# Kernel optimization log

Measured on AMD Instinct MI355X. Metric: run time of the kernel, lower is better.

## Reference

```python
import jax, jax.numpy as jnp
import numpy as np

B, N, C, H = 8, 2048, 512, 8
D = C // H  # head_dim = 64

def rope(t):
    # t: (B, H, T, D); rotate even/odd interleaved pairs
    T = t.shape[2]
    inv_freq = 1.0 / (10000.0 ** (jnp.arange(0, D, 2, dtype=t.dtype) / D))  # (D/2,)
    pos = jnp.arange(T, dtype=t.dtype)
    freqs = pos[:, None] * inv_freq[None, :]            # (T, D/2)
    cos, sin = jnp.cos(freqs), jnp.sin(freqs)           # broadcast over (B,H)
    t_un = t[..., 0::2]
    t_ev = t[..., 1::2]
    r_un = t_un * cos - t_ev * sin
    r_ev = t_un * sin + t_ev * cos
    # interleave back: (..., D/2, 2) -> (..., D)
    return jnp.stack([r_un, r_ev], axis=-1).reshape(t.shape)

def setup_inputs() -> dict:
    key = jax.random.key(0)
    k1, k2, k3, k4 = jax.random.split(key, 4)
    x = jax.random.normal(k1, (B, N, C), dtype=jnp.float32)
    mask = jax.random.normal(k2, (B, N), dtype=jnp.float32)
    W_qkv = jax.random.normal(k3, (3 * C, C), dtype=jnp.float32) * (1.0 / np.sqrt(C))
    W_proj = jax.random.normal(k4, (C, C), dtype=jnp.float32) * (1.0 / np.sqrt(C))
    b_proj = jnp.zeros((C,), dtype=jnp.float32)
    return {"x": x, "mask": mask, "W_qkv": W_qkv, "W_proj": W_proj,
            "b_proj": b_proj, "num_cls_token": 1}

def reference(x, mask, W_qkv, W_proj, b_proj, num_cls_token):
    scale = D ** (-0.5)
    qkv = jnp.einsum('bnc,fc->bnf', x, W_qkv)             # (B,N,3C)
    qkv = qkv.reshape(B, N, 3, H, D).transpose(2, 0, 3, 1, 4)  # (3,B,H,N,D)
    q, k, v = qkv[0], qkv[1], qkv[2]
    nc = num_cls_token
    if nc > 0:
        q = jnp.concatenate([q[:, :, :nc], rope(q[:, :, nc:])], axis=2)
        k = jnp.concatenate([k[:, :, :nc], rope(k[:, :, nc:])], axis=2)
    else:
        q, k = rope(q), rope(k)
    attn = jnp.einsum('bhnd,bhmd->bhnm', q * scale, k)    # (B,H,N,N)
    attn = attn + mask[:, None, None, :] + mask[:, None, :, None]
    attn = jax.nn.softmax(attn, axis=-1)
    out = jnp.einsum('bhnm,bhmd->bhnd', attn, v)          # (B,H,N,D)
    out = out.transpose(0, 2, 1, 3).reshape(B, N, C)
    return out @ W_proj.T + b_proj
```

## Files before the change

kernel.cpp:

```cpp
#include <hip/hip_runtime.h>
#include <cmath>

#define BB 8
#define NN 2048
#define CC 512
#define HH 8
#define DD 64
#define FF 1536
#define MM (BB*NN)

typedef _Float16 half_t;
typedef __attribute__((ext_vector_type(8))) _Float16 half8;
typedef __attribute__((ext_vector_type(4))) _Float16 half4;
typedef __attribute__((ext_vector_type(4))) float floatx4;

#define LOG2E 1.44269504088896f

typedef const __attribute__((address_space(1))) unsigned int* gas_ptr;
typedef __attribute__((address_space(3))) unsigned int* las_ptr;
__device__ __forceinline__ void gld16(const half_t* g, half_t* l) {
  __builtin_amdgcn_global_load_lds((gas_ptr)g, (las_ptr)l, 16, 0, 0);
}

__global__ __launch_bounds__(256) void cvt_kernel(
    const float* __restrict__ s, half_t* __restrict__ d, int n8) {
  int i = blockIdx.x * 256 + threadIdx.x;
  if (i < n8) {
    float4 a = ((const float4*)s)[i * 2], b = ((const float4*)s)[i * 2 + 1];
    half8 h;
    h[0] = (half_t)a.x; h[1] = (half_t)a.y; h[2] = (half_t)a.z; h[3] = (half_t)a.w;
    h[4] = (half_t)b.x; h[5] = (half_t)b.y; h[6] = (half_t)b.z; h[7] = (half_t)b.w;
    ((half8*)d)[i] = h;
  }
}

__global__ __launch_bounds__(256) void qkv_mfma_kernel(
    const half_t* __restrict__ Ah,
    const half_t* __restrict__ Bh,
    const int*   __restrict__ ncp,
    half_t* __restrict__ Qh, half_t* __restrict__ Kh, half_t* __restrict__ Vt)
{
  __shared__ union {
    struct { half_t A[128 * 32]; half_t B[128 * 32]; } s;
    half_t T[4][64 * 68];
  } sm;

  const int tid  = threadIdx.x;
  const int wave = tid >> 6, lane = tid & 63;
  const int L15  = lane & 15, quad = lane >> 4;
  const int wm = (wave & 1) * 64, wn = (wave >> 1) * 64;
  const int m0 = blockIdx.x * 128;
  const int f0 = blockIdx.y * 128;

  const int srow = lane >> 2;
  const int scolh = (lane & 3) * 8;
  const half_t* Ag = Ah + (size_t)(m0 + wave * 16 + srow) * CC + scolh;
  const half_t* Bg = Bh + (size_t)(f0 + wave * 16 + srow) * CC + scolh;
  half_t* Al = &sm.s.A[(wave * 16) * 32];
  half_t* Bl = &sm.s.B[(wave * 16) * 32];

  floatx4 acc[4][4];
#pragma unroll
  for (int i = 0; i < 4; ++i)
#pragma unroll
    for (int j = 0; j < 4; ++j) acc[i][j] = (floatx4){0.f, 0.f, 0.f, 0.f};

  for (int k0 = 0; k0 < CC; k0 += 32) {
    __syncthreads();
    gld16(Ag + k0,            Al);
    gld16(Ag + k0 + 64 * CC,  Al + 64 * 32);
    gld16(Bg + k0,            Bl);
    gld16(Bg + k0 + 64 * CC,  Bl + 64 * 32);
    __syncthreads();
    half8 af[4], bf[4];
#pragma unroll
    for (int mi = 0; mi < 4; ++mi)
      af[mi] = *(const half8*)&sm.s.A[(wm + mi * 16 + L15) * 32 + quad * 8];
#pragma unroll
    for (int ni = 0; ni < 4; ++ni)
      bf[ni] = *(const half8*)&sm.s.B[(wn + ni * 16 + L15) * 32 + quad * 8];
#pragma unroll
    for (int mi = 0; mi < 4; ++mi)
#pragma unroll
      for (int ni = 0; ni < 4; ++ni)
        acc[mi][ni] = __builtin_amdgcn_mfma_f32_16x16x32_f16(af[mi], bf[ni], acc[mi][ni], 0, 0, 0);
  }

  const int which = f0 >> 9;
  const int b     = m0 >> 11;
  const int n_base = (m0 & 2047) + wm;

  if (which < 2) {
    const int nc = *ncp;
    half_t* dst = which ? Kh : Qh;
    const float qscale = which ? 1.0f : (0.125f * LOG2E);
#pragma unroll
    for (int ni = 0; ni < 4; ++ni) {
      const int f = f0 + wn + ni * 16 + L15;
      const int h = (f >> 6) & 7;
      const int d = f & 63;
      const float invf = __powf(10000.0f, -(float)(d & ~1) * (1.0f / 64.0f));
      const float sgn = (d & 1) ? 1.0f : -1.0f;
#pragma unroll
      for (int mi = 0; mi < 4; ++mi)
#pragma unroll
        for (int r = 0; r < 4; ++r) {
          const int n = n_base + mi * 16 + quad * 4 + r;
          float v = acc[mi][ni][r];
          float p = __shfl_xor(v, 1, 64);
          if (n >= nc) {
            float sv, cv;
            __sincosf((float)(n - nc) * invf, &sv, &cv);
            v = v * cv + sgn * p * sv;
          }
          dst[(((size_t)(b * HH + h) * NN + n) << 6) + d] = (half_t)(v * qscale);
        }
    }
  } else {
    __syncthreads();
#pragma unroll
    for (int ni = 0; ni < 4; ++ni)
#pragma unroll
      for (int mi = 0; mi < 4; ++mi)
#pragma unroll
        for (int r = 0; r < 4; ++r)
          sm.T[wave][(ni * 16 + L15) * 68 + mi * 16 + quad * 4 + r] = (half_t)acc[mi][ni][r];
    __syncthreads();
    const int h = ((f0 + wn) >> 6) & 7;
    const size_t gbase = ((size_t)(b * HH + h) * DD + lane) * NN + n_base;
#pragma unroll
    for (int c = 0; c < 8; ++c)
      *(half8*)(Vt + gbase + c * 8) = *(const half8*)&sm.T[wave][lane * 68 + c * 8];
  }
}

#define KPAD 72
#define PPAD 68
#define EXP2_OFF 4.3280851f
__global__ __launch_bounds__(256, 4) void flash_mfma_kernel(
    const half_t* __restrict__ Qh,
    const half_t* __restrict__ Kh,
    const half_t* __restrict__ Vt,
    const float*  __restrict__ mask,
    half_t* __restrict__ O)
{
  __shared__ half_t Ks[64 * KPAD];
  __shared__ half_t Vs[64 * KPAD];
  __shared__ half_t Ps[4][32 * PPAD];

  const int tid  = threadIdx.x;
  const int wave = tid >> 6;
  const int lane = tid & 63;
  const int L15  = lane & 15;
  const int quad = lane >> 4;

  const int bid  = blockIdx.x;
  const int xcd  = bid & 7;
  const int slot = bid >> 3;
  const int qt   = slot & 15;
  const int head = (slot >> 4) * 8 + xcd;
  const int b    = head >> 3;
  const int h    = head & 7;

  const half_t* Kt_base = Kh + ((((size_t)b * HH + h) * NN) << 6);
  const half_t* Vt_base = Vt + ((((size_t)b * HH + h) * DD) * NN);

  half8 qa[2][2];
#pragma unroll
  for (int g = 0; g < 2; ++g) {
    const half_t* Qrow =
        Qh + ((((size_t)b * HH + h) * NN + qt * 128 + wave * 32 + g * 16 + L15) << 6);
    qa[g][0] = *(const half8*)(Qrow + quad * 8);
    qa[g][1] = *(const half8*)(Qrow + 32 + quad * 8);
  }

  floatx4 oacc[2][4];
#pragma unroll
  for (int g = 0; g < 2; ++g)
#pragma unroll
    for (int sd = 0; sd < 4; ++sd) oacc[g][sd] = (floatx4){0.f, 0.f, 0.f, 0.f};
  float l_part[2][4] = {};

  const int sn = tid >> 3;
  const int sp = (tid & 7) * 8;
  half8 kreg[2], vreg[2];
  float mk_cur[4], mk_nxt[4];
#define LOAD_KV(kt)                                                               \
  {                                                                               \
    kreg[0] = *(const half8*)(Kt_base + (((size_t)(kt) * 64 + sn) << 6) + sp);    \
    kreg[1] = *(const half8*)(Kt_base + (((size_t)(kt) * 64 + sn + 32) << 6) + sp); \
    vreg[0] = *(const half8*)(Vt_base + (size_t)sn * NN + (kt) * 64 + sp);        \
    vreg[1] = *(const half8*)(Vt_base + (size_t)(sn + 32) * NN + (kt) * 64 + sp); \
  }
#define LOAD_MK(kt, dstm)                                                         \
  {                                                                               \
    _Pragma("unroll")                                                             \
    for (int s = 0; s < 4; ++s)                                                   \
      dstm[s] = mask[(size_t)b * NN + (kt) * 64 + s * 16 + L15] * LOG2E - EXP2_OFF; \
  }

  LOAD_KV(0)
  LOAD_MK(0, mk_cur)

  for (int kt = 0; kt < NN / 64; ++kt) {
    __syncthreads();
    *(half8*)&Ks[sn * KPAD + sp]        = kreg[0];
    *(half8*)&Ks[(sn + 32) * KPAD + sp] = kreg[1];
    *(half8*)&Vs[sn * KPAD + sp]        = vreg[0];
    *(half8*)&Vs[(sn + 32) * KPAD + sp] = vreg[1];
    __syncthreads();
    if (kt + 1 < NN / 64) {
      LOAD_KV(kt + 1)
      LOAD_MK(kt + 1, mk_nxt)
    }

    floatx4 S[2][4];
#pragma unroll
    for (int s = 0; s < 4; ++s) {
      half8 kb0 = *(const half8*)&Ks[(s * 16 + L15) * KPAD + quad * 8];
      half8 kb1 = *(const half8*)&Ks[(s * 16 + L15) * KPAD + 32 + quad * 8];
#pragma unroll
      for (int g = 0; g < 2; ++g) {
        floatx4 a = (floatx4){0.f, 0.f, 0.f, 0.f};
        a = __builtin_amdgcn_mfma_f32_16x16x32_f16(qa[g][0], kb0, a, 0, 0, 0);
        a = __builtin_amdgcn_mfma_f32_16x16x32_f16(qa[g][1], kb1, a, 0, 0, 0);
        S[g][s] = a;
      }
    }

#pragma unroll
    for (int g = 0; g < 2; ++g)
#pragma unroll
      for (int s = 0; s < 4; ++s)
#pragma unroll
        for (int r = 0; r < 4; ++r) {
          float p = __builtin_amdgcn_exp2f(S[g][s][r] + mk_cur[s]);
          l_part[g][r] += p;
          Ps[wave][(g * 16 + quad * 4 + r) * PPAD + s * 16 + L15] = (half_t)p;
        }

    half8 pa[2][2];
#pragma unroll
    for (int g = 0; g < 2; ++g) {
      pa[g][0] = *(const half8*)&Ps[wave][(g * 16 + L15) * PPAD + quad * 8];
      pa[g][1] = *(const half8*)&Ps[wave][(g * 16 + L15) * PPAD + 32 + quad * 8];
    }

#pragma unroll
    for (int sd = 0; sd < 4; ++sd) {
      half8 vb0 = *(const half8*)&Vs[(sd * 16 + L15) * KPAD + quad * 8];
      half8 vb1 = *(const half8*)&Vs[(sd * 16 + L15) * KPAD + 32 + quad * 8];
#pragma unroll
      for (int g = 0; g < 2; ++g) {
        oacc[g][sd] = __builtin_amdgcn_mfma_f32_16x16x32_f16(pa[g][0], vb0, oacc[g][sd], 0, 0, 0);
        oacc[g][sd] = __builtin_amdgcn_mfma_f32_16x16x32_f16(pa[g][1], vb1, oacc[g][sd], 0, 0, 0);
      }
    }

#pragma unroll
    for (int s = 0; s < 4; ++s) mk_cur[s] = mk_nxt[s];
  }

#pragma unroll
  for (int g = 0; g < 2; ++g)
#pragma unroll
    for (int r = 0; r < 4; ++r) {
#pragma unroll
      for (int off = 1; off < 16; off <<= 1)
        l_part[g][r] += __shfl_xor(l_part[g][r], off, 64);
    }

#pragma unroll
  for (int g = 0; g < 2; ++g)
#pragma unroll
    for (int r = 0; r < 4; ++r) {
      const float invl = 1.0f / l_part[g][r];
      const int row = qt * 128 + wave * 32 + g * 16 + quad * 4 + r;
#pragma unroll
      for (int sd = 0; sd < 4; ++sd)
        O[(((size_t)b * NN + row) << 9) + (h << 6) + sd * 16 + L15] =
            (half_t)(oacc[g][sd][r] * invl);
    }
}

__global__ __launch_bounds__(256) void proj_mfma_kernel(
    const half_t* __restrict__ Ah,
    const half_t* __restrict__ Bh,
    const float* __restrict__ bias,
    float* __restrict__ out)
{
  __shared__ half_t As[128 * 32];
  __shared__ half_t Bs[128 * 32];

  const int tid  = threadIdx.x;
  const int wave = tid >> 6, lane = tid & 63;
  const int L15  = lane & 15, quad = lane >> 4;
  const int wm = (wave & 1) * 64, wn = (wave >> 1) * 64;
  const int m0 = blockIdx.x * 128;
  const int f0 = blockIdx.y * 128;

  const int srow = lane >> 2;
  const int scolh = (lane & 3) * 8;
  const half_t* Ag = Ah + (size_t)(m0 + wave * 16 + srow) * CC + scolh;
  const half_t* Bg = Bh + (size_t)(f0 + wave * 16 + srow) * CC + scolh;
  half_t* Al = &As[(wave * 16) * 32];
  half_t* Bl = &Bs[(wave * 16) * 32];

  floatx4 acc[4][4];
#pragma unroll
  for (int i = 0; i < 4; ++i)
#pragma unroll
    for (int j = 0; j < 4; ++j) acc[i][j] = (floatx4){0.f, 0.f, 0.f, 0.f};

  for (int k0 = 0; k0 < CC; k0 += 32) {
    __syncthreads();
    gld16(Ag + k0,           Al);
    gld16(Ag + k0 + 64 * CC, Al + 64 * 32);
    gld16(Bg + k0,           Bl);
    gld16(Bg + k0 + 64 * CC, Bl + 64 * 32);
    __syncthreads();
    half8 af[4], bf[4];
#pragma unroll
    for (int mi = 0; mi < 4; ++mi)
      af[mi] = *(const half8*)&As[(wm + mi * 16 + L15) * 32 + quad * 8];
#pragma unroll
    for (int ni = 0; ni < 4; ++ni)
      bf[ni] = *(const half8*)&Bs[(wn + ni * 16 + L15) * 32 + quad * 8];
#pragma unroll
    for (int mi = 0; mi < 4; ++mi)
#pragma unroll
      for (int ni = 0; ni < 4; ++ni)
        acc[mi][ni] = __builtin_amdgcn_mfma_f32_16x16x32_f16(af[mi], bf[ni], acc[mi][ni], 0, 0, 0);
  }

#pragma unroll
  for (int ni = 0; ni < 4; ++ni) {
    const int f = f0 + wn + ni * 16 + L15;
    const float bv = bias[f];
#pragma unroll
    for (int mi = 0; mi < 4; ++mi)
#pragma unroll
      for (int r = 0; r < 4; ++r)
        out[(size_t)(m0 + wm + mi * 16 + quad * 4 + r) * CC + f] = acc[mi][ni][r] + bv;
  }
}

extern "C" void kernel_launch(void* const* d_in, const int* in_sizes, int n_in,
                              void* d_out, int out_size, void* d_ws, size_t ws_size,
                              hipStream_t stream) {
  const float* x     = (const float*)d_in[0];
  const float* mask  = (const float*)d_in[1];
  const float* Wqkv  = (const float*)d_in[2];
  const float* Wproj = (const float*)d_in[3];
  const float* bproj = (const float*)d_in[4];
  const int*   ncp   = (const int*)d_in[5];
  float* out = (float*)d_out;

  const size_t per = (size_t)BB * HH * NN * DD;
  half_t* xh  = (half_t*)d_ws;
  half_t* Wqh = xh + (size_t)MM * CC;
  half_t* Wph = Wqh + (size_t)FF * CC;
  half_t* Qh  = Wph + (size_t)CC * CC;
  half_t* Kh  = Qh + per;
  half_t* Vt  = Kh + per;
  half_t* Oh  = Vt + per;

  cvt_kernel<<<dim3(MM * CC / 8 / 256), 256, 0, stream>>>(x, xh, MM * CC / 8);
  cvt_kernel<<<dim3(FF * CC / 8 / 256), 256, 0, stream>>>(Wqkv, Wqh, FF * CC / 8);
  cvt_kernel<<<dim3(CC * CC / 8 / 256), 256, 0, stream>>>(Wproj, Wph, CC * CC / 8);

  qkv_mfma_kernel<<<dim3(MM / 128, FF / 128), 256, 0, stream>>>(xh, Wqh, ncp, Qh, Kh, Vt);
  flash_mfma_kernel<<<dim3(BB * HH * (NN / 128)), 256, 0, stream>>>(Qh, Kh, Vt, mask, Oh);
  proj_mfma_kernel<<<dim3(MM / 128, CC / 128), 256, 0, stream>>>(Oh, Wph, bproj, out);
}
```

Baseline: 266.9 us.

## Load K/V fragments directly from global and precompute exp-mask factors

The flash kernel no longer stages K and V tiles through shared memory with block-wide barriers. Each wave now loads its MFMA operands straight from global memory, relying on L2/L1 reuse across the four waves. The key-mask is precomputed once as a half-precision exp2 factor in a new small kernel and multiplied into exp2(S), replacing a per-element add. The MFMA operand order is swapped to transpose the S and O tiles, which gives vectorized P stores and output writes. Occupancy hint drops from 4 to 3 blocks. This removes barriers and LDS traffic but duplicates global loads per wave, and storing the mask factor in fp16 may cost some precision.

```diff
diff --git a/kernel.cpp b/kernel.cpp
--- a/kernel.cpp
+++ b/kernel.cpp
@@ -15,6 +15,7 @@
 typedef __attribute__((ext_vector_type(4))) float floatx4;
 
 #define LOG2E 1.44269504088896f
+#define EXP2_OFF 4.3280851f
 
 typedef const __attribute__((address_space(1))) unsigned int* gas_ptr;
 typedef __attribute__((address_space(3))) unsigned int* las_ptr;
@@ -32,6 +33,13 @@
     h[4] = (half_t)b.x; h[5] = (half_t)b.y; h[6] = (half_t)b.z; h[7] = (half_t)b.w;
     ((half8*)d)[i] = h;
   }
+}
+
+__global__ __launch_bounds__(256) void em_kernel(
+    const float* __restrict__ mask, half_t* __restrict__ EM, int n) {
+  int i = blockIdx.x * 256 + threadIdx.x;
+  if (i < n)
+    EM[i] = (half_t)__builtin_amdgcn_exp2f(mask[i] * LOG2E - EXP2_OFF);
 }
 
 __global__ __launch_bounds__(256) void qkv_mfma_kernel(
@@ -134,19 +142,15 @@
   }
 }
 
-#define KPAD 72
-#define PPAD 68
-#define EXP2_OFF 4.3280851f
-__global__ __launch_bounds__(256, 4) void flash_mfma_kernel(
+#define PP 72
+__global__ __launch_bounds__(256, 3) void flash_mfma_kernel(
     const half_t* __restrict__ Qh,
     const half_t* __restrict__ Kh,
     const half_t* __restrict__ Vt,
-    const float*  __restrict__ mask,
+    const half_t* __restrict__ EM,
     half_t* __restrict__ O)
 {
-  __shared__ half_t Ks[64 * KPAD];
-  __shared__ half_t Vs[64 * KPAD];
-  __shared__ half_t Ps[4][32 * PPAD];
+  __shared__ half_t Pst[4][32 * PP];
 
   const int tid  = threadIdx.x;
   const int wave = tid >> 6;
@@ -164,6 +168,7 @@
 
   const half_t* Kt_base = Kh + ((((size_t)b * HH + h) * NN) << 6);
   const half_t* Vt_base = Vt + ((((size_t)b * HH + h) * DD) * NN);
+  const half_t* EMb     = EM + (size_t)b * NN;
 
   half8 qa[2][2];
 #pragma unroll
@@ -179,108 +184,98 @@
   for (int g = 0; g < 2; ++g)
 #pragma unroll
     for (int sd = 0; sd < 4; ++sd) oacc[g][sd] = (floatx4){0.f, 0.f, 0.f, 0.f};
-  float l_part[2][4] = {};
-
-  const int sn = tid >> 3;
-  const int sp = (tid & 7) * 8;
-  half8 kreg[2], vreg[2];
-  float mk_cur[4], mk_nxt[4];
-#define LOAD_KV(kt)                                                               \
-  {                                                                               \
-    kreg[0] = *(const half8*)(Kt_base + (((size_t)(kt) * 64 + sn) << 6) + sp);    \
-    kreg[1] = *(const half8*)(Kt_base + (((size_t)(kt) * 64 + sn + 32) << 6) + sp); \
-    vreg[0] = *(const half8*)(Vt_base + (size_t)sn * NN + (kt) * 64 + sp);        \
-    vreg[1] = *(const half8*)(Vt_base + (size_t)(sn + 32) * NN + (kt) * 64 + sp); \
-  }
-#define LOAD_MK(kt, dstm)                                                         \
-  {                                                                               \
-    _Pragma("unroll")                                                             \
-    for (int s = 0; s < 4; ++s)                                                   \
-      dstm[s] = mask[(size_t)b * NN + (kt) * 64 + s * 16 + L15] * LOG2E - EXP2_OFF; \
-  }
-
-  LOAD_KV(0)
-  LOAD_MK(0, mk_cur)
+  float l_part[2] = {0.f, 0.f};
+
+  half_t* Pw = &Pst[wave][0];
 
   for (int kt = 0; kt < NN / 64; ++kt) {
-    __syncthreads();
-    *(half8*)&Ks[sn * KPAD + sp]        = kreg[0];
-    *(half8*)&Ks[(sn + 32) * KPAD + sp] = kreg[1];
-    *(half8*)&Vs[sn * KPAD + sp]        = vreg[0];
-    *(half8*)&Vs[(sn + 32) * KPAD + sp] = vreg[1];
-    __syncthreads();
-    if (kt + 1 < NN / 64) {
-      LOAD_KV(kt + 1)
-      LOAD_MK(kt + 1, mk_nxt)
-    }
+    half8 ka[4][2];
+#pragma unroll
+    for (int s = 0; s < 4; ++s) {
+      const half_t* kr = Kt_base + (((size_t)kt * 64 + s * 16 + L15) << 6) + quad * 8;
+      ka[s][0] = *(const half8*)(kr);
+      ka[s][1] = *(const half8*)(kr + 32);
+    }
+    half4 em4[4];
+#pragma unroll
+    for (int s = 0; s < 4; ++s)
+      em4[s] = *(const half4*)(EMb + kt * 64 + s * 16 + quad * 4);
 
     floatx4 S[2][4];
 #pragma unroll
-    for (int s = 0; s < 4; ++s) {
-      half8 kb0 = *(const half8*)&Ks[(s * 16 + L15) * KPAD + quad * 8];
-      half8 kb1 = *(const half8*)&Ks[(s * 16 + L15) * KPAD + 32 + quad * 8];
+    for (int s = 0; s < 4; ++s)
 #pragma unroll
       for (int g = 0; g < 2; ++g) {
         floatx4 a = (floatx4){0.f, 0.f, 0.f, 0.f};
-        a = __builtin_amdgcn_mfma_f32_16x16x32_f16(qa[g][0], kb0, a, 0, 0, 0);
-        a = __builtin_amdgcn_mfma_f32_16x16x32_f16(qa[g][1], kb1, a, 0, 0, 0);
+        a = __builtin_amdgcn_mfma_f32_16x16x32_f16(ka[s][0], qa[g][0], a, 0, 0, 0);
+        a = __builtin_amdgcn_mfma_f32_16x16x32_f16(ka[s][1], qa[g][1], a, 0, 0, 0);
         S[g][s] = a;
       }
-    }
-
+
+    half8 vb[4][2];
+#pragma unroll
+    for (int sd = 0; sd < 4; ++sd) {
+      const half_t* vr = Vt_base + (size_t)(sd * 16 + L15) * NN + kt * 64 + quad * 8;
+      vb[sd][0] = *(const half8*)(vr);
+      vb[sd][1] = *(const half8*)(vr + 32);
+    }
+
+#pragma unroll
+    for (int s = 0; s < 4; ++s) {
+      float emf0 = (float)em4[s][0], emf1 = (float)em4[s][1];
+      float emf2 = (float)em4[s][2], emf3 = (float)em4[s][3];
+#pragma unroll
+      for (int g = 0; g < 2; ++g) {
+        float p0 = __builtin_amdgcn_exp2f(S[g][s][0]);
+        float p1 = __builtin_amdgcn_exp2f(S[g][s][1]);
+        float p2 = __builtin_amdgcn_exp2f(S[g][s][2]);
+        float p3 = __builtin_amdgcn_exp2f(S[g][s][3]);
+        l_part[g] += p0 * emf0 + p1 * emf1 + p2 * emf2 + p3 * emf3;
+        half4 pv = {(half_t)(p0 * emf0), (half_t)(p1 * emf1),
+                    (half_t)(p2 * emf2), (half_t)(p3 * emf3)};
+        *(half4*)&Pw[(g * 16 + L15) * PP + s * 16 + quad * 4] = pv;
+      }
+    }
+
+    __asm__ volatile("s_waitcnt lgkmcnt(0)" ::: "memory");
+
+    half8 pa[2][2];
 #pragma unroll
     for (int g = 0; g < 2; ++g)
 #pragma unroll
-      for (int s = 0; s < 4; ++s)
-#pragma unroll
-        for (int r = 0; r < 4; ++r) {
-          float p = __builtin_amdgcn_exp2f(S[g][s][r] + mk_cur[s]);
-          l_part[g][r] += p;
-          Ps[wave][(g * 16 + quad * 4 + r) * PPAD + s * 16 + L15] = (half_t)p;
-        }
-
-    half8 pa[2][2];
-#pragma unroll
-    for (int g = 0; g < 2; ++g) {
-      pa[g][0] = *(const half8*)&Ps[wave][(g * 16 + L15) * PPAD + quad * 8];
-      pa[g][1] = *(const half8*)&Ps[wave][(g * 16 + L15) * PPAD + 32 + quad * 8];
-    }
-
+      for (int c = 0; c < 2; ++c) {
+        half4 lo = *(const half4*)&Pw[(g * 16 + L15) * PP + c * 32 + quad * 8];
+        half4 hi = *(const half4*)&Pw[(g * 16 + L15) * PP + c * 32 + quad * 8 + 4];
+        pa[g][c] = __builtin_shufflevector(lo, hi, 0, 1, 2, 3, 4, 5, 6, 7);
+      }
+
+#pragma unroll
+    for (int sd = 0; sd < 4; ++sd)
+#pragma unroll
+      for (int g = 0; g < 2; ++g) {
+        oacc[g][sd] = __builtin_amdgcn_mfma_f32_16x16x32_f16(vb[sd][0], pa[g][0], oacc[g][sd], 0, 0, 0);
+        oacc[g][sd] = __builtin_amdgcn_mfma_f32_16x16x32_f16(vb[sd][1], pa[g][1], oacc[g][sd], 0, 0, 0);
+      }
+  }
+
+#pragma unroll
+  for (int g = 0; g < 2; ++g) {
+    l_part[g] += __shfl_xor(l_part[g], 16, 64);
+    l_part[g] += __shfl_xor(l_part[g], 32, 64);
+  }
+
+#pragma unroll
+  for (int g = 0; g < 2; ++g) {
+    const float invl = 1.0f / l_part[g];
+    const int row = qt * 128 + wave * 32 + g * 16 + L15;
+    half_t* ob = O + (((size_t)b * NN + row) << 9) + (h << 6);
 #pragma unroll
     for (int sd = 0; sd < 4; ++sd) {
-      half8 vb0 = *(const half8*)&Vs[(sd * 16 + L15) * KPAD + quad * 8];
-      half8 vb1 = *(const half8*)&Vs[(sd * 16 + L15) * KPAD + 32 + quad * 8];
-#pragma unroll
-      for (int g = 0; g < 2; ++g) {
-        oacc[g][sd] = __builtin_amdgcn_mfma_f32_16x16x32_f16(pa[g][0], vb0, oacc[g][sd], 0, 0, 0);
-        oacc[g][sd] = __builtin_amdgcn_mfma_f32_16x16x32_f16(pa[g][1], vb1, oacc[g][sd], 0, 0, 0);
-      }
-    }
-
-#pragma unroll
-    for (int s = 0; s < 4; ++s) mk_cur[s] = mk_nxt[s];
-  }
-
-#pragma unroll
-  for (int g = 0; g < 2; ++g)
-#pragma unroll
-    for (int r = 0; r < 4; ++r) {
-#pragma unroll
-      for (int off = 1; off < 16; off <<= 1)
-        l_part[g][r] += __shfl_xor(l_part[g][r], off, 64);
-    }
-
-#pragma unroll
-  for (int g = 0; g < 2; ++g)
-#pragma unroll
-    for (int r = 0; r < 4; ++r) {
-      const float invl = 1.0f / l_part[g][r];
-      const int row = qt * 128 + wave * 32 + g * 16 + quad * 4 + r;
-#pragma unroll
-      for (int sd = 0; sd < 4; ++sd)
-        O[(((size_t)b * NN + row) << 9) + (h << 6) + sd * 16 + L15] =
-            (half_t)(oacc[g][sd][r] * invl);
-    }
+      half4 o4 = {(half_t)(oacc[g][sd][0] * invl), (half_t)(oacc[g][sd][1] * invl),
+                  (half_t)(oacc[g][sd][2] * invl), (half_t)(oacc[g][sd][3] * invl)};
+      *(half4*)(ob + sd * 16 + quad * 4) = o4;
+    }
+  }
 }
 
 __global__ __launch_bounds__(256) void proj_mfma_kernel(
@@ -364,12 +359,14 @@
   half_t* Kh  = Qh + per;
   half_t* Vt  = Kh + per;
   half_t* Oh  = Vt + per;
+  half_t* EMt = Oh + (size_t)MM * CC;
 
   cvt_kernel<<<dim3(MM * CC / 8 / 256), 256, 0, stream>>>(x, xh, MM * CC / 8);
   cvt_kernel<<<dim3(FF * CC / 8 / 256), 256, 0, stream>>>(Wqkv, Wqh, FF * CC / 8);
   cvt_kernel<<<dim3(CC * CC / 8 / 256), 256, 0, stream>>>(Wproj, Wph, CC * CC / 8);
+  em_kernel<<<dim3(MM / 256), 256, 0, stream>>>(mask, EMt, MM);
 
   qkv_mfma_kernel<<<dim3(MM / 128, FF / 128), 256, 0, stream>>>(xh, Wqh, ncp, Qh, Kh, Vt);
-  flash_mfma_kernel<<<dim3(BB * HH * (NN / 128)), 256, 0, stream>>>(Qh, Kh, Vt, mask, Oh);
+  flash_mfma_kernel<<<dim3(BB * HH * (NN / 128)), 256, 0, stream>>>(Qh, Kh, Vt, EMt, Oh);
   proj_mfma_kernel<<<dim3(MM / 128, CC / 128), 256, 0, stream>>>(Oh, Wph, bproj, out);
 }
```

Result: slower. 438.8 us (+64.4%).
